# Kernel optimization log

Measured on AMD Instinct MI355X. Metric: run time of the kernel, lower is better.

Reference implementation:

```python
import jax, jax.numpy as jnp
import numpy as np

FEATURE_DIM = 256
NUM_HASHES = 128
NUM_NODES = 500000
NUM_SEGMENTS = 512


def setup_inputs() -> dict:
    key = jax.random.key(0)
    k_x, k_b, k_h = jax.random.split(key, 3)
    x = jax.random.normal(k_x, (NUM_NODES, FEATURE_DIM), dtype=jnp.float32)
    batch = jnp.sort(jax.random.randint(k_b, (NUM_NODES,), 0, NUM_SEGMENTS, dtype=jnp.int64))
    hash_matrices = jax.random.normal(k_h, (NUM_HASHES, FEATURE_DIM), dtype=jnp.float32)
    return {"x": x, "batch": batch, "num_segments": NUM_SEGMENTS, "hash_matrices": hash_matrices}


def reference(x, batch, num_segments, hash_matrices):
    # hash_values: [num_nodes, num_hashes]
    hash_values = jnp.matmul(x, hash_matrices.T)
    # per-graph (segment) min over nodes -> [num_segments, num_hashes]
    sketch = jax.ops.segment_min(hash_values, batch, num_segments=num_segments)
    # torch leaves empty groups at zero; empty segments come back +inf here
    sketch = jnp.where(jnp.isinf(sketch), jnp.zeros_like(sketch), sketch)
    return sketch
```

## Files before the change

kernel.cpp:

```cpp
#include <hip/hip_runtime.h>


#define M_NODES 500000
#define KDIM    256
#define NHASH   128
#define NSEG    512

#define BM     128
#define BK     32
#define NCHUNK (KDIM / BK)

typedef __attribute__((ext_vector_type(8))) short bf16x8;
typedef __attribute__((ext_vector_type(4))) float f32x4;

__device__ __forceinline__ unsigned short f2bf(float f) {
    unsigned int u = __float_as_uint(f);
    u += 0x7FFFu + ((u >> 16) & 1u);
    return (unsigned short)(u >> 16);
}
__device__ __forceinline__ float bf2f(unsigned short s) {
    return __uint_as_float(((unsigned int)s) << 16);
}
__device__ __forceinline__ unsigned int enc_f(float f) {
    unsigned int b = __float_as_uint(f);
    return (b & 0x80000000u) ? ~b : (b | 0x80000000u);
}

__global__ void hsplit(const float* __restrict__ H,
                       unsigned short* __restrict__ b1f,
                       unsigned short* __restrict__ b2f) {
    const int t = blockIdx.x * 256 + threadIdx.x;
    const int n = t >> 8;
    const int k = t & 255;
    const float h = H[t];
    const unsigned short s1 = f2bf(h);
    const unsigned short s2 = f2bf(h - bf2f(s1));
    const int idx = ((k >> 5) * 8 + (n >> 4)) * 512 + (((k >> 3) & 3) * 16 + (n & 15)) * 8 + (k & 7);
    b1f[idx] = s1;
    b2f[idx] = s2;
}

#define ATILE 576
#define AKG   144

__global__ __launch_bounds__(256, 3)
void minhash_main(const float* __restrict__ x,
                  const unsigned int* __restrict__ batch_raw,
                  const unsigned short* __restrict__ b1f,
                  const unsigned short* __restrict__ b2f,
                  unsigned int* __restrict__ ws) {
    __shared__ __align__(16) char smem[34816];
    unsigned short* a1 = (unsigned short*)smem;
    unsigned short* a2 = a1 + 4608;
    unsigned short* b1 = a1 + 9216;
    unsigned short* b2 = a1 + 13312;
    float* sc = (float*)smem;

    const int tid  = threadIdx.x;
    const int lane = tid & 63;
    const int w    = __builtin_amdgcn_readfirstlane(tid >> 6);
    const int quad = lane >> 4;
    const int c16  = lane & 15;
    const int rh   = w & 1;
    const int ch   = w >> 1;
    const long long blockBase = (long long)blockIdx.x * BM;

    f32x4 acc[4][4];
    #pragma unroll
    for (int rt = 0; rt < 4; ++rt)
        #pragma unroll
        for (int ct = 0; ct < 4; ++ct)
            acc[rt][ct] = (f32x4){0.f, 0.f, 0.f, 0.f};

    for (int chunk = 0; chunk < NCHUNK; ++chunk) {
        const int k0 = chunk * BK;

        {
            const float4* gb1 = (const float4*)(b1f + chunk * 4096);
            const float4* gb2 = (const float4*)(b2f + chunk * 4096);
            ((float4*)b1)[tid]       = gb1[tid];
            ((float4*)b1)[tid + 256] = gb1[tid + 256];
            ((float4*)b2)[tid]       = gb2[tid];
            ((float4*)b2)[tid + 256] = gb2[tid + 256];
        }
        #pragma unroll
        for (int pass = 0; pass < 4; ++pass) {
            const int r  = (tid >> 3) + pass * 32;
            const int f4 = tid & 7;
            const long long gr = blockBase + r;
            float4 vv = make_float4(0.f, 0.f, 0.f, 0.f);
            if (gr < (long long)M_NODES)
                vv = *(const float4*)(x + gr * KDIM + k0 + f4 * 4);
            const unsigned short h1x = f2bf(vv.x), h1y = f2bf(vv.y),
                                 h1z = f2bf(vv.z), h1w = f2bf(vv.w);
            const unsigned short l1x = f2bf(vv.x - bf2f(h1x)), l1y = f2bf(vv.y - bf2f(h1y)),
                                 l1z = f2bf(vv.z - bf2f(h1z)), l1w = f2bf(vv.w - bf2f(h1w));
            const int base = (r >> 4) * ATILE + (f4 >> 1) * AKG + (r & 15) * 8 + (f4 & 1) * 4;
            uint2 p1, p2;
            p1.x = (unsigned)h1x | ((unsigned)h1y << 16);
            p1.y = (unsigned)h1z | ((unsigned)h1w << 16);
            p2.x = (unsigned)l1x | ((unsigned)l1y << 16);
            p2.y = (unsigned)l1z | ((unsigned)l1w << 16);
            *(uint2*)(a1 + base) = p1;
            *(uint2*)(a2 + base) = p2;
        }
        __syncthreads();

        bf16x8 a1f[4], a2f[4];
        #pragma unroll
        for (int rt = 0; rt < 4; ++rt) {
            const int off = (rh * 4 + rt) * ATILE + quad * AKG + c16 * 8;
            a1f[rt] = *(const bf16x8*)(a1 + off);
            a2f[rt] = *(const bf16x8*)(a2 + off);
        }
        #pragma unroll
        for (int ct = 0; ct < 4; ++ct) {
            const int boff = ((ch * 4 + ct) * 64 + lane) * 8;
            const bf16x8 b1v = *(const bf16x8*)(b1 + boff);
            const bf16x8 b2v = *(const bf16x8*)(b2 + boff);
            #pragma unroll
            for (int rt = 0; rt < 4; ++rt) {
                acc[rt][ct] = __builtin_amdgcn_mfma_f32_16x16x32_bf16(a1f[rt], b1v, acc[rt][ct], 0, 0, 0);
                acc[rt][ct] = __builtin_amdgcn_mfma_f32_16x16x32_bf16(a2f[rt], b1v, acc[rt][ct], 0, 0, 0);
                acc[rt][ct] = __builtin_amdgcn_mfma_f32_16x16x32_bf16(a1f[rt], b2v, acc[rt][ct], 0, 0, 0);
                acc[rt][ct] = __builtin_amdgcn_mfma_f32_16x16x32_bf16(a2f[rt], b2v, acc[rt][ct], 0, 0, 0);
            }
        }
        __syncthreads();
    }

    const bool is64 = (batch_raw[499999] == 0u);
    const long long* bb64 = (const long long*)batch_raw;
    const int*       bb32 = (const int*)batch_raw;

    const int p = lane;
    const int cg = w;
    const long long gn0 = blockBase + 2 * p;
    const long long gn1 = gn0 + 1;
    int seg0 = -1, seg1 = -1;
    if (gn0 < (long long)M_NODES) seg0 = is64 ? (int)bb64[gn0] : bb32[gn0];
    if (gn1 < (long long)M_NODES) seg1 = is64 ? (int)bb64[gn1] : bb32[gn1];

    for (int h = 0; h < 2; ++h) {
        if (ch == h) {
            #pragma unroll
            for (int ct = 0; ct < 4; ++ct) {
                #pragma unroll
                for (int rt = 0; rt < 4; ++rt) {
                    const int node = rh * 64 + rt * 16 + quad * 4;
                    const int colp = ct * 16 + c16;
                    *(f32x4*)(sc + colp * 132 + node) = acc[rt][ct];
                }
            }
        }
        __syncthreads();

        float v[16];
        int seg;
        if (seg0 == seg1) {
            seg = seg0;
            #pragma unroll
            for (int j = 0; j < 16; ++j) {
                const float2 nv = *(const float2*)(sc + (cg * 16 + j) * 132 + 2 * p);
                v[j] = fminf(nv.x, nv.y);
            }
        } else {
            seg = seg1;
            #pragma unroll
            for (int j = 0; j < 16; ++j) {
                const float2 nv = *(const float2*)(sc + (cg * 16 + j) * 132 + 2 * p);
                if (seg0 >= 0)
                    atomicMin(&ws[seg0 * NHASH + h * 64 + cg * 16 + j], enc_f(nv.x));
                v[j] = nv.y;
            }
        }
        #pragma unroll
        for (int d = 1; d < 64; d <<= 1) {
            const int  oseg = __shfl_down(seg, d, 64);
            const bool ok   = (lane + d < 64) && (oseg == seg);
            #pragma unroll
            for (int j = 0; j < 16; ++j) {
                const float ov = __shfl_down(v[j], d, 64);
                if (ok) v[j] = fminf(v[j], ov);
            }
        }
        const int pseg = __shfl_up(seg, 1, 64);
        if (seg >= 0 && (lane == 0 || pseg != seg)) {
            #pragma unroll
            for (int j = 0; j < 16; ++j)
                atomicMin(&ws[seg * NHASH + h * 64 + cg * 16 + j], enc_f(v[j]));
        }
        __syncthreads();
    }
}

__global__ void minhash_finalize(const unsigned int* __restrict__ ws,
                                 float* __restrict__ out) {
    const int i = blockIdx.x * blockDim.x + threadIdx.x;
    if (i < NSEG * NHASH) {
        const unsigned int u = ws[i];
        out[i] = (u == 0xFFFFFFFFu)
                     ? 0.0f
                     : ((u & 0x80000000u) ? __uint_as_float(u ^ 0x80000000u)
                                          : __uint_as_float(~u));
    }
}

extern "C" void kernel_launch(void* const* d_in, const int* in_sizes, int n_in,
                              void* d_out, int out_size, void* d_ws, size_t ws_size,
                              hipStream_t stream) {
    const float* x = (const float*)d_in[0];
    const unsigned int* batch = (const unsigned int*)d_in[1];
    const float* H = (const float*)d_in[3];

    unsigned int*   ws  = (unsigned int*)d_ws;
    unsigned short* b1f = (unsigned short*)((char*)d_ws + 256 * 1024);
    unsigned short* b2f = (unsigned short*)((char*)d_ws + 320 * 1024);

    hipMemsetAsync(d_ws, 0xFF, NSEG * NHASH * sizeof(unsigned int), stream);
    hsplit<<<(KDIM * NHASH) / 256, 256, 0, stream>>>(H, b1f, b2f);

    const int grid = (M_NODES + BM - 1) / BM;
    minhash_main<<<grid, 256, 0, stream>>>(x, batch, b1f, b2f, ws);
    minhash_finalize<<<(NSEG * NHASH + 255) / 256, 256, 0, stream>>>(ws, (float*)d_out);
}
```

Measured before the change: 730.6 us.

## Load x fragments directly into registers and drop LDS staging in GEMM loop

The GEMM main loop no longer stages A (split x) and B (split hash matrix) tiles through shared memory with two barriers per chunk. Each wave now owns 32 rows across all 128 hashes, loads its x fragments straight from global memory into MFMA operand layout with a one-chunk register prefetch, splits them to hi/lo bf16 in registers, and reads B fragments directly from the pre-swizzled global buffer, relying on cache. This is meant to remove LDS traffic and sync stalls. In exchange, each wave re-reads B from global/L2 and the x loads are less coalesced (32-byte pieces per lane), with more accumulator registers per thread.

```diff
diff --git a/kernel.cpp b/kernel.cpp
--- a/kernel.cpp
+++ b/kernel.cpp
@@ -24,6 +24,18 @@
 __device__ __forceinline__ unsigned int enc_f(float f) {
     unsigned int b = __float_as_uint(f);
     return (b & 0x80000000u) ? ~b : (b | 0x80000000u);
+}
+
+__device__ __forceinline__ void split8(const float4& A, const float4& B,
+                                       bf16x8& hi, bf16x8& lo) {
+    const unsigned short h0 = f2bf(A.x), h1 = f2bf(A.y), h2 = f2bf(A.z), h3 = f2bf(A.w);
+    const unsigned short h4 = f2bf(B.x), h5 = f2bf(B.y), h6 = f2bf(B.z), h7 = f2bf(B.w);
+    hi = (bf16x8){(short)h0, (short)h1, (short)h2, (short)h3,
+                  (short)h4, (short)h5, (short)h6, (short)h7};
+    lo = (bf16x8){(short)f2bf(A.x - bf2f(h0)), (short)f2bf(A.y - bf2f(h1)),
+                  (short)f2bf(A.z - bf2f(h2)), (short)f2bf(A.w - bf2f(h3)),
+                  (short)f2bf(B.x - bf2f(h4)), (short)f2bf(B.y - bf2f(h5)),
+                  (short)f2bf(B.z - bf2f(h6)), (short)f2bf(B.w - bf2f(h7))};
 }
 
 __global__ void hsplit(const float* __restrict__ H,
@@ -40,93 +52,72 @@
     b2f[idx] = s2;
 }
 
-#define ATILE 576
-#define AKG   144
-
 __global__ __launch_bounds__(256, 3)
 void minhash_main(const float* __restrict__ x,
                   const unsigned int* __restrict__ batch_raw,
                   const unsigned short* __restrict__ b1f,
                   const unsigned short* __restrict__ b2f,
                   unsigned int* __restrict__ ws) {
-    __shared__ __align__(16) char smem[34816];
-    unsigned short* a1 = (unsigned short*)smem;
-    unsigned short* a2 = a1 + 4608;
-    unsigned short* b1 = a1 + 9216;
-    unsigned short* b2 = a1 + 13312;
-    float* sc = (float*)smem;
+    __shared__ __align__(16) float sc[8448];
 
     const int tid  = threadIdx.x;
     const int lane = tid & 63;
     const int w    = __builtin_amdgcn_readfirstlane(tid >> 6);
     const int quad = lane >> 4;
     const int c16  = lane & 15;
-    const int rh   = w & 1;
-    const int ch   = w >> 1;
     const long long blockBase = (long long)blockIdx.x * BM;
 
-    f32x4 acc[4][4];
+    const long long r0 = blockBase + w * 32 + c16;
+    const long long r1 = r0 + 16;
+    const bool g0 = r0 < (long long)M_NODES;
+    const bool g1 = r1 < (long long)M_NODES;
+    const float* pa0 = x + r0 * KDIM + quad * 8;
+    const float* pa1 = x + r1 * KDIM + quad * 8;
+
+    f32x4 acc[2][8];
     #pragma unroll
-    for (int rt = 0; rt < 4; ++rt)
-        #pragma unroll
-        for (int ct = 0; ct < 4; ++ct)
-            acc[rt][ct] = (f32x4){0.f, 0.f, 0.f, 0.f};
+    for (int rt = 0; rt < 2; ++rt)
+        #pragma unroll
+        for (int nt = 0; nt < 8; ++nt)
+            acc[rt][nt] = (f32x4){0.f, 0.f, 0.f, 0.f};
+
+    const float4 z4 = make_float4(0.f, 0.f, 0.f, 0.f);
+    float4 n0a = g0 ? *(const float4*)(pa0)     : z4;
+    float4 n0b = g0 ? *(const float4*)(pa0 + 4) : z4;
+    float4 n1a = g1 ? *(const float4*)(pa1)     : z4;
+    float4 n1b = g1 ? *(const float4*)(pa1 + 4) : z4;
+
+    const unsigned short* gb1 = b1f + lane * 8;
+    const unsigned short* gb2 = b2f + lane * 8;
 
     for (int chunk = 0; chunk < NCHUNK; ++chunk) {
-        const int k0 = chunk * BK;
-
-        {
-            const float4* gb1 = (const float4*)(b1f + chunk * 4096);
-            const float4* gb2 = (const float4*)(b2f + chunk * 4096);
-            ((float4*)b1)[tid]       = gb1[tid];
-            ((float4*)b1)[tid + 256] = gb1[tid + 256];
-            ((float4*)b2)[tid]       = gb2[tid];
-            ((float4*)b2)[tid + 256] = gb2[tid + 256];
-        }
-        #pragma unroll
-        for (int pass = 0; pass < 4; ++pass) {
-            const int r  = (tid >> 3) + pass * 32;
-            const int f4 = tid & 7;
-            const long long gr = blockBase + r;
-            float4 vv = make_float4(0.f, 0.f, 0.f, 0.f);
-            if (gr < (long long)M_NODES)
-                vv = *(const float4*)(x + gr * KDIM + k0 + f4 * 4);
-            const unsigned short h1x = f2bf(vv.x), h1y = f2bf(vv.y),
-                                 h1z = f2bf(vv.z), h1w = f2bf(vv.w);
-            const unsigned short l1x = f2bf(vv.x - bf2f(h1x)), l1y = f2bf(vv.y - bf2f(h1y)),
-                                 l1z = f2bf(vv.z - bf2f(h1z)), l1w = f2bf(vv.w - bf2f(h1w));
-            const int base = (r >> 4) * ATILE + (f4 >> 1) * AKG + (r & 15) * 8 + (f4 & 1) * 4;
-            uint2 p1, p2;
-            p1.x = (unsigned)h1x | ((unsigned)h1y << 16);
-            p1.y = (unsigned)h1z | ((unsigned)h1w << 16);
-            p2.x = (unsigned)l1x | ((unsigned)l1y << 16);
-            p2.y = (unsigned)l1z | ((unsigned)l1w << 16);
-            *(uint2*)(a1 + base) = p1;
-            *(uint2*)(a2 + base) = p2;
-        }
-        __syncthreads();
-
-        bf16x8 a1f[4], a2f[4];
-        #pragma unroll
-        for (int rt = 0; rt < 4; ++rt) {
-            const int off = (rh * 4 + rt) * ATILE + quad * AKG + c16 * 8;
-            a1f[rt] = *(const bf16x8*)(a1 + off);
-            a2f[rt] = *(const bf16x8*)(a2 + off);
-        }
-        #pragma unroll
-        for (int ct = 0; ct < 4; ++ct) {
-            const int boff = ((ch * 4 + ct) * 64 + lane) * 8;
-            const bf16x8 b1v = *(const bf16x8*)(b1 + boff);
-            const bf16x8 b2v = *(const bf16x8*)(b2 + boff);
-            #pragma unroll
-            for (int rt = 0; rt < 4; ++rt) {
-                acc[rt][ct] = __builtin_amdgcn_mfma_f32_16x16x32_bf16(a1f[rt], b1v, acc[rt][ct], 0, 0, 0);
-                acc[rt][ct] = __builtin_amdgcn_mfma_f32_16x16x32_bf16(a2f[rt], b1v, acc[rt][ct], 0, 0, 0);
-                acc[rt][ct] = __builtin_amdgcn_mfma_f32_16x16x32_bf16(a1f[rt], b2v, acc[rt][ct], 0, 0, 0);
-                acc[rt][ct] = __builtin_amdgcn_mfma_f32_16x16x32_bf16(a2f[rt], b2v, acc[rt][ct], 0, 0, 0);
-            }
-        }
-        __syncthreads();
+        const float4 c0a = n0a, c0b = n0b, c1a = n1a, c1b = n1b;
+        if (chunk < NCHUNK - 1) {
+            const int o = (chunk + 1) * BK;
+            n0a = g0 ? *(const float4*)(pa0 + o)     : z4;
+            n0b = g0 ? *(const float4*)(pa0 + o + 4) : z4;
+            n1a = g1 ? *(const float4*)(pa1 + o)     : z4;
+            n1b = g1 ? *(const float4*)(pa1 + o + 4) : z4;
+        }
+        bf16x8 a1_0, a2_0, a1_1, a2_1;
+        split8(c0a, c0b, a1_0, a2_0);
+        split8(c1a, c1b, a1_1, a2_1);
+
+        const unsigned short* cb1 = gb1 + chunk * 4096;
+        const unsigned short* cb2 = gb2 + chunk * 4096;
+        #pragma unroll
+        for (int nt = 0; nt < 8; ++nt) {
+            const bf16x8 b1v = *(const bf16x8*)(cb1 + nt * 512);
+            const bf16x8 b2v = *(const bf16x8*)(cb2 + nt * 512);
+            acc[0][nt] = __builtin_amdgcn_mfma_f32_16x16x32_bf16(a1_0, b1v, acc[0][nt], 0, 0, 0);
+            acc[0][nt] = __builtin_amdgcn_mfma_f32_16x16x32_bf16(a2_0, b1v, acc[0][nt], 0, 0, 0);
+            acc[0][nt] = __builtin_amdgcn_mfma_f32_16x16x32_bf16(a1_0, b2v, acc[0][nt], 0, 0, 0);
+            acc[0][nt] = __builtin_amdgcn_mfma_f32_16x16x32_bf16(a2_0, b2v, acc[0][nt], 0, 0, 0);
+            acc[1][nt] = __builtin_amdgcn_mfma_f32_16x16x32_bf16(a1_1, b1v, acc[1][nt], 0, 0, 0);
+            acc[1][nt] = __builtin_amdgcn_mfma_f32_16x16x32_bf16(a2_1, b1v, acc[1][nt], 0, 0, 0);
+            acc[1][nt] = __builtin_amdgcn_mfma_f32_16x16x32_bf16(a1_1, b2v, acc[1][nt], 0, 0, 0);
+            acc[1][nt] = __builtin_amdgcn_mfma_f32_16x16x32_bf16(a2_1, b2v, acc[1][nt], 0, 0, 0);
+        }
     }
 
     const bool is64 = (batch_raw[499999] == 0u);
@@ -141,16 +132,15 @@
     if (gn0 < (long long)M_NODES) seg0 = is64 ? (int)bb64[gn0] : bb32[gn0];
     if (gn1 < (long long)M_NODES) seg1 = is64 ? (int)bb64[gn1] : bb32[gn1];
 
+    #pragma unroll
     for (int h = 0; h < 2; ++h) {
-        if (ch == h) {
-            #pragma unroll
-            for (int ct = 0; ct < 4; ++ct) {
-                #pragma unroll
-                for (int rt = 0; rt < 4; ++rt) {
-                    const int node = rh * 64 + rt * 16 + quad * 4;
-                    const int colp = ct * 16 + c16;
-                    *(f32x4*)(sc + colp * 132 + node) = acc[rt][ct];
-                }
+        #pragma unroll
+        for (int ct = 0; ct < 4; ++ct) {
+            #pragma unroll
+            for (int rt = 0; rt < 2; ++rt) {
+                const int node = w * 32 + rt * 16 + quad * 4;
+                const int colp = ct * 16 + c16;
+                *(f32x4*)(sc + colp * 132 + node) = acc[rt][h * 4 + ct];
             }
         }
         __syncthreads();
```

Result: slower. 750.3 us (+2.7%).

## Prefetch next x chunk into registers and double-buffer B via LDS DMA

Applied to the files above, without the earlier changes.

The K-chunk loop becomes a software pipeline. While the current chunk is converted and multiplied, the next chunk of x is loaded into registers. The hash-matrix tiles are copied into a double-buffered LDS region with global_load_lds, so the fetch no longer stalls before each chunk. The plain __syncthreads is replaced by a barrier that only waits on lgkmcnt, and correctness of the async LDS copy relies on the in-order vmcnt wait forced by the register loads. LDS use grows to 50 KB per block, which may limit how many blocks fit on a CU.

```diff
diff --git a/kernel.cpp b/kernel.cpp
--- a/kernel.cpp
+++ b/kernel.cpp
@@ -43,17 +43,23 @@
 #define ATILE 576
 #define AKG   144
 
+__device__ __forceinline__ void barrier_lgkm() {
+    __builtin_amdgcn_sched_barrier(0);
+    asm volatile("s_waitcnt lgkmcnt(0)" ::: "memory");
+    __builtin_amdgcn_s_barrier();
+    __builtin_amdgcn_sched_barrier(0);
+}
+
 __global__ __launch_bounds__(256, 3)
 void minhash_main(const float* __restrict__ x,
                   const unsigned int* __restrict__ batch_raw,
                   const unsigned short* __restrict__ b1f,
                   const unsigned short* __restrict__ b2f,
                   unsigned int* __restrict__ ws) {
-    __shared__ __align__(16) char smem[34816];
+    __shared__ __align__(16) char smem[51200];
     unsigned short* a1 = (unsigned short*)smem;
     unsigned short* a2 = a1 + 4608;
-    unsigned short* b1 = a1 + 9216;
-    unsigned short* b2 = a1 + 13312;
+    unsigned short* bb = a1 + 9216;
     float* sc = (float*)smem;
 
     const int tid  = threadIdx.x;
@@ -65,6 +71,9 @@
     const int ch   = w >> 1;
     const long long blockBase = (long long)blockIdx.x * BM;
 
+    const int arow = tid >> 3;
+    const int f4   = tid & 7;
+
     f32x4 acc[4][4];
     #pragma unroll
     for (int rt = 0; rt < 4; ++rt)
@@ -72,25 +81,30 @@
         for (int ct = 0; ct < 4; ++ct)
             acc[rt][ct] = (f32x4){0.f, 0.f, 0.f, 0.f};
 
-    for (int chunk = 0; chunk < NCHUNK; ++chunk) {
-        const int k0 = chunk * BK;
-
-        {
-            const float4* gb1 = (const float4*)(b1f + chunk * 4096);
-            const float4* gb2 = (const float4*)(b2f + chunk * 4096);
-            ((float4*)b1)[tid]       = gb1[tid];
-            ((float4*)b1)[tid + 256] = gb1[tid + 256];
-            ((float4*)b2)[tid]       = gb2[tid];
-            ((float4*)b2)[tid + 256] = gb2[tid + 256];
-        }
-        #pragma unroll
-        for (int pass = 0; pass < 4; ++pass) {
-            const int r  = (tid >> 3) + pass * 32;
-            const int f4 = tid & 7;
-            const long long gr = blockBase + r;
-            float4 vv = make_float4(0.f, 0.f, 0.f, 0.f);
-            if (gr < (long long)M_NODES)
-                vv = *(const float4*)(x + gr * KDIM + k0 + f4 * 4);
+    const float4 z4 = make_float4(0.f, 0.f, 0.f, 0.f);
+
+    #pragma unroll
+    for (int s = 0; s < 2; ++s)
+        #pragma unroll
+        for (int j = 0; j < 2; ++j) {
+            const unsigned short* src = (s ? b2f : b1f) + (w * 2 + j) * 512 + lane * 8;
+            unsigned short* dst = bb + s * 4096 + (w * 2 + j) * 512;
+            __builtin_amdgcn_global_load_lds(
+                (const __attribute__((address_space(1))) unsigned int*)src,
+                (__attribute__((address_space(3))) unsigned int*)dst, 16, 0, 0);
+        }
+    float4 av[4];
+    #pragma unroll
+    for (int p = 0; p < 4; ++p) {
+        const long long gr = blockBase + arow + p * 32;
+        av[p] = (gr < (long long)M_NODES) ? *(const float4*)(x + gr * KDIM + f4 * 4) : z4;
+    }
+
+    for (int c = 0; c < NCHUNK; ++c) {
+        #pragma unroll
+        for (int p = 0; p < 4; ++p) {
+            const int r = arow + p * 32;
+            const float4 vv = av[p];
             const unsigned short h1x = f2bf(vv.x), h1y = f2bf(vv.y),
                                  h1z = f2bf(vv.z), h1w = f2bf(vv.w);
             const unsigned short l1x = f2bf(vv.x - bf2f(h1x)), l1y = f2bf(vv.y - bf2f(h1y)),
@@ -104,7 +118,26 @@
             *(uint2*)(a1 + base) = p1;
             *(uint2*)(a2 + base) = p2;
         }
-        __syncthreads();
+        if (c < NCHUNK - 1) {
+            const int cn = c + 1;
+            #pragma unroll
+            for (int s = 0; s < 2; ++s)
+                #pragma unroll
+                for (int j = 0; j < 2; ++j) {
+                    const unsigned short* src = (s ? b2f : b1f) + cn * 4096 + (w * 2 + j) * 512 + lane * 8;
+                    unsigned short* dst = bb + (cn & 1) * 8192 + s * 4096 + (w * 2 + j) * 512;
+                    __builtin_amdgcn_global_load_lds(
+                        (const __attribute__((address_space(1))) unsigned int*)src,
+                        (__attribute__((address_space(3))) unsigned int*)dst, 16, 0, 0);
+                }
+            #pragma unroll
+            for (int p = 0; p < 4; ++p) {
+                const long long gr = blockBase + arow + p * 32;
+                av[p] = (gr < (long long)M_NODES)
+                            ? *(const float4*)(x + gr * KDIM + cn * BK + f4 * 4) : z4;
+            }
+        }
+        barrier_lgkm();
 
         bf16x8 a1f[4], a2f[4];
         #pragma unroll
@@ -113,11 +146,12 @@
             a1f[rt] = *(const bf16x8*)(a1 + off);
             a2f[rt] = *(const bf16x8*)(a2 + off);
         }
+        const unsigned short* bcur = bb + (c & 1) * 8192;
         #pragma unroll
         for (int ct = 0; ct < 4; ++ct) {
             const int boff = ((ch * 4 + ct) * 64 + lane) * 8;
-            const bf16x8 b1v = *(const bf16x8*)(b1 + boff);
-            const bf16x8 b2v = *(const bf16x8*)(b2 + boff);
+            const bf16x8 b1v = *(const bf16x8*)(bcur + boff);
+            const bf16x8 b2v = *(const bf16x8*)(bcur + 4096 + boff);
             #pragma unroll
             for (int rt = 0; rt < 4; ++rt) {
                 acc[rt][ct] = __builtin_amdgcn_mfma_f32_16x16x32_bf16(a1f[rt], b1v, acc[rt][ct], 0, 0, 0);
@@ -126,7 +160,7 @@
                 acc[rt][ct] = __builtin_amdgcn_mfma_f32_16x16x32_bf16(a2f[rt], b2v, acc[rt][ct], 0, 0, 0);
             }
         }
-        __syncthreads();
+        barrier_lgkm();
     }
 
     const bool is64 = (batch_raw[499999] == 0u);
```

Result: faster. 715.3 us (-2.1%).
